# Optimization experiments

Hardware: AMD Instinct MI355X
Metric: run time of the kernel (lower is better)

The kernel has to match this reference:

```python
import jax, jax.numpy as jnp
import numpy as np

HIDDEN = 1024
N_HEADS = 16
HEAD_DIM = HIDDEN // N_HEADS


def _rope_tables(seq_len, dim, dtype):
    inv_freq = 1.0 / (10000.0 ** (jnp.arange(0, dim, 2, dtype=jnp.float32) / dim))
    t = jnp.arange(seq_len, dtype=jnp.float32)
    freqs = jnp.einsum('i,j->ij', t, inv_freq)          # [S, dim/2]
    emb = jnp.concatenate([freqs, freqs], axis=-1)       # [S, dim]
    cos = jnp.cos(emb)[None, :, None, :].astype(dtype)   # [1, S, 1, dim]
    sin = jnp.sin(emb)[None, :, None, :].astype(dtype)
    return cos, sin


def _rotate_half(x):
    x1, x2 = x[..., : x.shape[-1] // 2], x[..., x.shape[-1] // 2 :]
    return jnp.concatenate([-x2, x1], axis=-1)


def setup_inputs() -> dict:
    key = jax.random.key(0)
    ks = jax.random.split(key, 9)
    s = 1.0 / np.sqrt(HIDDEN)
    return {
        'x': jax.random.normal(ks[0], (2, 2048, HIDDEN), dtype=jnp.float32),
        'q_w': jax.random.uniform(ks[1], (HIDDEN, HIDDEN), jnp.float32, -s, s),
        'q_b': jax.random.uniform(ks[2], (HIDDEN,), jnp.float32, -s, s),
        'k_w': jax.random.uniform(ks[3], (HIDDEN, HIDDEN), jnp.float32, -s, s),
        'k_b': jax.random.uniform(ks[4], (HIDDEN,), jnp.float32, -s, s),
        'v_w': jax.random.uniform(ks[5], (HIDDEN, HIDDEN), jnp.float32, -s, s),
        'v_b': jax.random.uniform(ks[6], (HIDDEN,), jnp.float32, -s, s),
        'o_w': jax.random.uniform(ks[7], (HIDDEN, HIDDEN), jnp.float32, -s, s),
        'o_b': jax.random.uniform(ks[8], (HIDDEN,), jnp.float32, -s, s),
    }


def reference(x, q_w, q_b, k_w, k_b, v_w, v_b, o_w, o_b):
    B, S, _ = x.shape
    scale = HEAD_DIM ** -0.5
    # projections (torch Linear: x @ W.T + b)
    q = (x @ q_w.T + q_b).reshape(B, S, N_HEADS, HEAD_DIM)
    k = (x @ k_w.T + k_b).reshape(B, S, N_HEADS, HEAD_DIM)
    v = (x @ v_w.T + v_b).reshape(B, S, N_HEADS, HEAD_DIM)
    # RoPE
    cos, sin = _rope_tables(S, HEAD_DIM, x.dtype)
    q = q * cos + _rotate_half(q) * sin
    k = k * cos + _rotate_half(k) * sin
    # attention: [B, H, S, S]
    scores = jnp.einsum('bqhd,bkhd->bhqk', q, k) * scale
    attn = jax.nn.softmax(scores, axis=-1)
    out = jnp.einsum('bhqk,bkhd->bqhd', attn, v).reshape(B, S, HIDDEN)
    return out @ o_w.T + o_b
```

## Files before the change

### kernel.cpp

```cpp
#include <hip/hip_runtime.h>
#include <hip/hip_bf16.h>


#define SEQ    2048
#define BATCH  2
#define NHEADS 16
#define HDIM   64
#define HID    1024
#define NTOK   (BATCH*SEQ)

typedef __bf16 bf16x8 __attribute__((ext_vector_type(8)));
typedef float  f32x4  __attribute__((ext_vector_type(4)));
typedef float  f32x16 __attribute__((ext_vector_type(16)));
typedef unsigned short u16x8 __attribute__((ext_vector_type(8)));
typedef unsigned int   u32x4 __attribute__((ext_vector_type(4)));

__device__ __forceinline__ unsigned short bfc(float x) {
  return __builtin_bit_cast(unsigned short, (__bf16)x);
}
__device__ __forceinline__ unsigned int pk(float lo, float hi) {
  return (unsigned int)bfc(lo) | ((unsigned int)bfc(hi) << 16);
}
__device__ __forceinline__ void plswap(unsigned int& a, unsigned int& b) {
  asm volatile("v_permlane32_swap_b32 %0, %1" : "+v"(a), "+v"(b));
}
#define EXP2(x) __builtin_amdgcn_exp2f(x)
#define MFMA32(a, b, c) __builtin_amdgcn_mfma_f32_32x32x16_bf16(a, b, c, 0, 0, 0)

__device__ __forceinline__ void gload16(const void* gptr, void* ldsptr) {
  typedef __attribute__((address_space(3))) unsigned int as3_uint;
  typedef const __attribute__((address_space(1))) unsigned int as1_uint;
  __builtin_amdgcn_global_load_lds(
      (as1_uint*)(unsigned long long)gptr,
      (as3_uint*)(unsigned int)(unsigned long long)ldsptr,
      16, 0, 0);
}

__device__ __forceinline__ void cvt8(const float* __restrict__ s,
                                     unsigned short* __restrict__ d, int i) {
  float4 a = *reinterpret_cast<const float4*>(s + i);
  float4 b = *reinterpret_cast<const float4*>(s + i + 4);
  u16x8 o;
  o[0] = bfc(a.x); o[1] = bfc(a.y); o[2] = bfc(a.z); o[3] = bfc(a.w);
  o[4] = bfc(b.x); o[5] = bfc(b.y); o[6] = bfc(b.z); o[7] = bfc(b.w);
  *reinterpret_cast<u16x8*>(d + i) = o;
}

__global__ __launch_bounds__(256) void prep(
    const float* __restrict__ x,
    const float* __restrict__ qw, const float* __restrict__ kw,
    const float* __restrict__ vw, const float* __restrict__ ow,
    unsigned short* __restrict__ xb,
    unsigned short* __restrict__ wqb, unsigned short* __restrict__ wkb,
    unsigned short* __restrict__ wvb, unsigned short* __restrict__ wob,
    float* __restrict__ ct, float* __restrict__ st)
{
  const int XN = NTOK * HID / 8;
  const int WN = HID * HID / 8;
  int tid = blockIdx.x * 256 + threadIdx.x;
  if (tid < XN) {
    cvt8(x, xb, tid * 8);
  } else if (tid < XN + 4 * WN) {
    int r = tid - XN;
    int which = r >> 17;
    int i = (r & (WN - 1)) * 8;
    const float* s = (which == 0) ? qw : (which == 1) ? kw : (which == 2) ? vw : ow;
    unsigned short* d = (which == 0) ? wqb : (which == 1) ? wkb : (which == 2) ? wvb : wob;
    cvt8(s, d, i);
  } else {
    int idx = tid - (XN + 4 * WN);
    if (idx < SEQ * 32) {
      int p = idx >> 5, j = idx & 31;
      float inv = powf(10000.0f, -(float)(2 * j) * (1.0f / 64.0f));
      float a = (float)p * inv;
      ct[idx] = cosf(a);
      st[idx] = sinf(a);
    }
  }
}

__global__ __launch_bounds__(256) void gemm_qkv(
    const unsigned short* __restrict__ X,
    const unsigned short* __restrict__ Wq, const unsigned short* __restrict__ Wk,
    const unsigned short* __restrict__ Wv,
    const float* __restrict__ bq, const float* __restrict__ bk, const float* __restrict__ bv,
    const float* __restrict__ ct, const float* __restrict__ st,
    unsigned short* __restrict__ Qo, unsigned short* __restrict__ Ko,
    unsigned short* __restrict__ VTo)
{
  __shared__ unsigned short LSH[24576];
  const int z = blockIdx.z;
  const unsigned short* W = (z == 0) ? Wq : (z == 1) ? Wk : Wv;
  const float* bias = (z == 0) ? bq : (z == 1) ? bk : bv;
  const int tm = blockIdx.x, tn = blockIdx.y;
  const int t = threadIdx.x, w = t >> 6, l = t & 63;
  const int wm = w >> 1, wn = w & 1, g = l >> 4;

  f32x4 acc[4][4] = {};

  const int arow0 = tm * 128, brow0 = tn * 128;
  const int s0 = w * 2, s1 = w * 2 + 1;
  const int r0 = s0 * 16 + (l >> 2), r1 = s1 * 16 + (l >> 2);
  const int kc = (l & 3) * 8;

#define GSTAGE(buf, k0)                                                               \
  {                                                                                   \
    gload16(X + (long)(arow0 + r0) * HID + (k0) + kc, LSH + (buf) * 4096 + s0 * 512); \
    gload16(X + (long)(arow0 + r1) * HID + (k0) + kc, LSH + (buf) * 4096 + s1 * 512); \
    gload16(W + (long)(brow0 + r0) * HID + (k0) + kc, LSH + 12288 + (buf) * 4096 + s0 * 512); \
    gload16(W + (long)(brow0 + r1) * HID + (k0) + kc, LSH + 12288 + (buf) * 4096 + s1 * 512); \
  }

  GSTAGE(0, 0)
  GSTAGE(1, 32)
  asm volatile("s_waitcnt vmcnt(4)" ::: "memory");
  __builtin_amdgcn_s_barrier();
  int cur = 0, stg = 2;
  for (int k0 = 0; k0 < HID; k0 += 32) {
    if (k0 + 64 < HID) GSTAGE(stg, k0 + 64)
    bf16x8 af[4], bfr[4];
#pragma unroll
    for (int fm = 0; fm < 4; ++fm)
      af[fm] = *reinterpret_cast<const bf16x8*>(
          LSH + cur * 4096 + (wm * 64 + fm * 16 + (l & 15)) * 32 + g * 8);
#pragma unroll
    for (int fn = 0; fn < 4; ++fn)
      bfr[fn] = *reinterpret_cast<const bf16x8*>(
          LSH + 12288 + cur * 4096 + (wn * 64 + fn * 16 + (l & 15)) * 32 + g * 8);
    __builtin_amdgcn_s_setprio(1);
#pragma unroll
    for (int fm = 0; fm < 4; ++fm)
#pragma unroll
      for (int fn = 0; fn < 4; ++fn)
        acc[fm][fn] = __builtin_amdgcn_mfma_f32_16x16x32_bf16(af[fm], bfr[fn], acc[fm][fn], 0, 0, 0);
    __builtin_amdgcn_s_setprio(0);
    if (k0 + 64 < HID) {
      asm volatile("s_waitcnt vmcnt(4)" ::: "memory");
    } else {
      asm volatile("s_waitcnt vmcnt(0)" ::: "memory");
    }
    __builtin_amdgcn_s_barrier();
    cur = (cur == 2) ? 0 : cur + 1;
    stg = (stg == 2) ? 0 : stg + 1;
  }
#undef GSTAGE

  const int colb = brow0 + wn * 64;
  float bsv[4];
#pragma unroll
  for (int fn = 0; fn < 4; ++fn) bsv[fn] = bias[colb + fn * 16 + (l & 15)];

  if (z == 2) {
#pragma unroll
    for (int fm = 0; fm < 4; ++fm) {
      int tok = wm * 64 + fm * 16 + g * 4;
#pragma unroll
      for (int fn = 0; fn < 4; ++fn) {
        int col = wn * 64 + fn * 16 + (l & 15);
        unsigned int u0 = (unsigned int)bfc(acc[fm][fn][0] + bsv[fn]) |
                          ((unsigned int)bfc(acc[fm][fn][1] + bsv[fn]) << 16);
        unsigned int u1 = (unsigned int)bfc(acc[fm][fn][2] + bsv[fn]) |
                          ((unsigned int)bfc(acc[fm][fn][3] + bsv[fn]) << 16);
        uint2 uv; uv.x = u0; uv.y = u1;
        *reinterpret_cast<uint2*>(&LSH[col * 128 + (tok ^ ((col & 7) << 3))]) = uv;
      }
    }
    __syncthreads();
    const int bb = arow0 >> 11, stok = arow0 & (SEQ - 1);
#pragma unroll
    for (int p8 = 0; p8 < 8; ++p8) {
      int col = p8 * 16 + (t >> 4);
      int soff = (t & 15) * 8;
      uint4 v = *reinterpret_cast<const uint4*>(&LSH[col * 128 + (soff ^ ((col & 7) << 3))]);
      int hh = (brow0 + col) >> 6;
      int dd = col & 63;
      unsigned short* dst = VTo + ((long)(bb * NHEADS + hh) * HDIM + dd) * SEQ + stok + soff;
      *reinterpret_cast<uint4*>(dst) = v;
    }
    return;
  }

  unsigned short* Out = (z == 0) ? Qo : Ko;
  const int h = colb >> 6;
#pragma unroll
  for (int fm = 0; fm < 4; ++fm) {
#pragma unroll
    for (int r = 0; r < 4; ++r) {
      int grow = arow0 + wm * 64 + fm * 16 + g * 4 + r;
      int b = grow >> 11, sidx = grow & (SEQ - 1);
      unsigned short* ob = Out + ((long)(b * NHEADS + h) * SEQ + sidx) * HDIM;
#pragma unroll
      for (int fn2 = 0; fn2 < 2; ++fn2) {
        int d1 = fn2 * 16 + (l & 15);
        float v1 = acc[fm][fn2][r] + bsv[fn2];
        float v2 = acc[fm][fn2 + 2][r] + bsv[fn2 + 2];
        float c = ct[sidx * 32 + d1], sn = st[sidx * 32 + d1];
        float o1 = v1 * c - v2 * sn;
        float o2 = v2 * c + v1 * sn;
        if (z == 0) { o1 *= 0.18033688f; o2 *= 0.18033688f; }
        ob[d1] = bfc(o1);
        ob[d1 + 32] = bfc(o2);
      }
    }
  }
}

__global__ __launch_bounds__(256, 2) void attn(
    const unsigned short* __restrict__ Qb,
    const unsigned short* __restrict__ Kb,
    const unsigned short* __restrict__ VTb,
    unsigned short* __restrict__ Ob)
{
  __shared__ unsigned short Kl[4][64 * 64];
  __shared__ unsigned short Vl[4][64 * 64];
  const int bh = blockIdx.x, qt = blockIdx.y;
  const int b = bh >> 4, h = bh & 15;
  const int t = threadIdx.x, w = t >> 6, l = t & 63;
  const long hb = (long)bh * SEQ * HDIM;
  const int hh = l >> 5;
  const int swz = (l & 7) << 4;

  const int q0 = qt * 128 + w * 32;
  bf16x8 qf[4];
#pragma unroll
  for (int dc = 0; dc < 4; ++dc)
    qf[dc] = *reinterpret_cast<const bf16x8*>(
        Qb + hb + (long)(q0 + (l & 31)) * HDIM + dc * 16 + hh * 8);

  f32x16 oacc[2] = {};
  f32x16 oaccE = {};
  const f32x16 FZ16 = {};

  u32x4 ou; ou[0] = 0x3F803F80u; ou[1] = 0x3F803F80u; ou[2] = 0x3F803F80u; ou[3] = 0x3F803F80u;
  const bf16x8 ones8 = __builtin_bit_cast(bf16x8, ou);

  const int srow = l >> 3;
  const int scol = (((l & 7) * 16) ^ ((l >> 3) << 4)) >> 1;
  const unsigned short* kp0 = Kb + hb + (long)(w * 16 + srow) * HDIM + scol;
  const unsigned short* kp1 = kp0 + 8 * HDIM;
  const unsigned short* vp0 = VTb + hb + (long)(w * 16 + srow) * SEQ + scol;
  const unsigned short* vp1 = vp0 + 8 * SEQ;

#define STAGE(buf)                                                     \
  {                                                                    \
    gload16(kp0, (char*)Kl + (buf) * 8192 + w * 2048);                 \
    gload16(kp1, (char*)Kl + (buf) * 8192 + w * 2048 + 1024);          \
    gload16(vp0, (char*)Vl + (buf) * 8192 + w * 2048);                 \
    gload16(vp1, (char*)Vl + (buf) * 8192 + w * 2048 + 1024);          \
    kp0 += 64 * HDIM; kp1 += 64 * HDIM; vp0 += 64; vp1 += 64;          \
  }

#define QK(kbuf)                                                                  \
  _Pragma("unroll")                                                               \
  for (int blk = 0; blk < 2; ++blk) {                                             \
    const char* kb_ = (char*)Kl + (kbuf) * 8192 + (32 * blk + (l & 31)) * 128;    \
    bf16x8 kf0 = *reinterpret_cast<const bf16x8*>(kb_ + ((0 * 32 + hh * 16) ^ swz)); \
    sa[blk] = MFMA32(kf0, qf[0], FZ16);                                           \
    bf16x8 kf1 = *reinterpret_cast<const bf16x8*>(kb_ + ((1 * 32 + hh * 16) ^ swz)); \
    sa[blk] = MFMA32(kf1, qf[1], sa[blk]);                                        \
    bf16x8 kf2 = *reinterpret_cast<const bf16x8*>(kb_ + ((2 * 32 + hh * 16) ^ swz)); \
    sa[blk] = MFMA32(kf2, qf[2], sa[blk]);                                        \
    bf16x8 kf3 = *reinterpret_cast<const bf16x8*>(kb_ + ((3 * 32 + hh * 16) ^ swz)); \
    sa[blk] = MFMA32(kf3, qf[3], sa[blk]);                                        \
  }

#define SOFTEXP                                                                   \
  _Pragma("unroll")                                                               \
  for (int blk = 0; blk < 2; ++blk)                                               \
    _Pragma("unroll")                                                             \
    for (int r = 0; r < 16; ++r) sa[blk][r] = EXP2(sa[blk][r]);

#define PBUILD                                                                    \
  _Pragma("unroll")                                                               \
  for (int blk = 0; blk < 2; ++blk) {                                             \
    unsigned int w0a = pk(sa[blk][0], sa[blk][1]);                                \
    unsigned int w1a = pk(sa[blk][2], sa[blk][3]);                                \
    unsigned int w0b = pk(sa[blk][4], sa[blk][5]);                                \
    unsigned int w1b = pk(sa[blk][6], sa[blk][7]);                                \
    unsigned int w0c = pk(sa[blk][8], sa[blk][9]);                                \
    unsigned int w1c = pk(sa[blk][10], sa[blk][11]);                              \
    unsigned int w0d = pk(sa[blk][12], sa[blk][13]);                              \
    unsigned int w1d = pk(sa[blk][14], sa[blk][15]);                              \
    plswap(w0a, w0b); plswap(w1a, w1b);                                           \
    plswap(w0c, w0d); plswap(w1c, w1d);                                           \
    u32x4 f0; f0[0] = w0a; f0[1] = w1a; f0[2] = w0b; f0[3] = w1b;                 \
    u32x4 f1; f1[0] = w0c; f1[1] = w1c; f1[2] = w0d; f1[3] = w1d;                 \
    pB[2 * blk + 0] = __builtin_bit_cast(bf16x8, f0);                             \
    pB[2 * blk + 1] = __builtin_bit_cast(bf16x8, f1);                             \
  }

#define PVSTEP(vbuf)                                                              \
  _Pragma("unroll")                                                               \
  for (int db = 0; db < 2; ++db) {                                                \
    const char* vb_ = (char*)Vl + (vbuf) * 8192 + (32 * db + (l & 31)) * 128;     \
    _Pragma("unroll")                                                             \
    for (int kc = 0; kc < 4; ++kc) {                                              \
      bf16x8 vf = *reinterpret_cast<const bf16x8*>(vb_ + ((kc * 32 + hh * 16) ^ swz)); \
      oacc[db] = MFMA32(vf, pB[kc], oacc[db]);                                    \
    }                                                                             \
  }                                                                               \
  _Pragma("unroll")                                                               \
  for (int kc = 0; kc < 4; ++kc) oaccE = MFMA32(ones8, pB[kc], oaccE);

#define ITER(KB, VR, SW)                                   \
  {                                                        \
    STAGE(SW)                                              \
    __builtin_amdgcn_s_setprio(1);                         \
    QK(KB)                                                 \
    PVSTEP(VR)                                             \
    __builtin_amdgcn_s_setprio(0);                         \
    SOFTEXP                                                \
    PBUILD                                                 \
    asm volatile("s_waitcnt vmcnt(4)" ::: "memory");       \
    __builtin_amdgcn_s_barrier();                          \
  }
#define ITER_DRAIN(KB, VR)                                 \
  {                                                        \
    __builtin_amdgcn_s_setprio(1);                         \
    QK(KB)                                                 \
    PVSTEP(VR)                                             \
    __builtin_amdgcn_s_setprio(0);                         \
    SOFTEXP                                                \
    PBUILD                                                 \
    asm volatile("s_waitcnt vmcnt(0)" ::: "memory");       \
    __builtin_amdgcn_s_barrier();                          \
  }
#define ITER_LAST(KB, VR)                                  \
  {                                                        \
    __builtin_amdgcn_s_setprio(1);                         \
    QK(KB)                                                 \
    PVSTEP(VR)                                             \
    __builtin_amdgcn_s_setprio(0);                         \
    SOFTEXP                                                \
    PBUILD                                                 \
  }

  f32x16 sa[2];
  bf16x8 pB[4];

  STAGE(0)
  STAGE(1)
  asm volatile("s_waitcnt vmcnt(4)" ::: "memory");
  __builtin_amdgcn_s_barrier();

  STAGE(2)
  __builtin_amdgcn_s_setprio(1);
  QK(0)
  __builtin_amdgcn_s_setprio(0);
  SOFTEXP
  PBUILD
  asm volatile("s_waitcnt vmcnt(4)" ::: "memory");
  __builtin_amdgcn_s_barrier();

  for (int m = 0; m < 7; ++m) {
    ITER(1, 0, 3)
    ITER(2, 1, 0)
    ITER(3, 2, 1)
    ITER(0, 3, 2)
  }
  ITER(1, 0, 3)
  ITER_DRAIN(2, 1)
  ITER_LAST(3, 2)

  __builtin_amdgcn_s_setprio(1);
  PVSTEP(3)
  __builtin_amdgcn_s_setprio(0);

#undef STAGE
#undef QK
#undef SOFTEXP
#undef PBUILD
#undef PVSTEP
#undef ITER
#undef ITER_DRAIN
#undef ITER_LAST

  {
    float inv = 1.0f / oaccE[0];
    int q = q0 + (l & 31);
    unsigned short* op = Ob + (long)(b * SEQ + q) * HID + h * HDIM;
#pragma unroll
    for (int db = 0; db < 2; ++db)
#pragma unroll
      for (int a = 0; a < 4; ++a) {
        int d = 8 * a + 4 * hh + 32 * db;
        unsigned int lo = pk(oacc[db][4 * a + 0] * inv, oacc[db][4 * a + 1] * inv);
        unsigned int hi2 = pk(oacc[db][4 * a + 2] * inv, oacc[db][4 * a + 3] * inv);
        uint2 uv; uv.x = lo; uv.y = hi2;
        *reinterpret_cast<uint2*>(op + d) = uv;
      }
  }
}

__global__ __launch_bounds__(256) void gemm_o(
    const unsigned short* __restrict__ A,
    const unsigned short* __restrict__ W,
    const float* __restrict__ bias,
    float* __restrict__ Out)
{
  __shared__ unsigned short Al[3][128 * 32];
  __shared__ unsigned short Bl[3][64 * 32];
  const int tm = blockIdx.x, tn = blockIdx.y;
  const int t = threadIdx.x, w = t >> 6, l = t & 63;
  const int wm = w >> 1, wn = w & 1;

  f32x4 acc[4][2] = {};
  const int arow0 = tm * 128, brow0 = tn * 64;
  const int s0 = w * 2, s1 = w * 2 + 1;
  const int r0 = s0 * 16 + (l >> 2), r1 = s1 * 16 + (l >> 2);
  const int rb = w * 16 + (l >> 2);
  const int kc = (l & 3) * 8;

#define GSTAGE(buf, k0)                                                       \
  {                                                                           \
    gload16(A + (long)(arow0 + r0) * HID + (k0) + kc, Al[buf] + s0 * 512);    \
    gload16(A + (long)(arow0 + r1) * HID + (k0) + kc, Al[buf] + s1 * 512);    \
    gload16(W + (long)(brow0 + rb) * HID + (k0) + kc, Bl[buf] + w * 512);     \
  }

  GSTAGE(0, 0)
  GSTAGE(1, 32)
  asm volatile("s_waitcnt vmcnt(3)" ::: "memory");
  __builtin_amdgcn_s_barrier();
  int cur = 0, stg = 2;
  for (int k0 = 0; k0 < HID; k0 += 32) {
    if (k0 + 64 < HID) GSTAGE(stg, k0 + 64)
    bf16x8 af[4], bfr[2];
#pragma unroll
    for (int fm = 0; fm < 4; ++fm)
      af[fm] = *reinterpret_cast<const bf16x8*>(Al[cur] + (wm * 64 + fm * 16 + (l & 15)) * 32 + (l >> 4) * 8);
#pragma unroll
    for (int fn = 0; fn < 2; ++fn)
      bfr[fn] = *reinterpret_cast<const bf16x8*>(Bl[cur] + (wn * 32 + fn * 16 + (l & 15)) * 32 + (l >> 4) * 8);
    __builtin_amdgcn_s_setprio(1);
#pragma unroll
    for (int fm = 0; fm < 4; ++fm)
#pragma unroll
      for (int fn = 0; fn < 2; ++fn)
        acc[fm][fn] = __builtin_amdgcn_mfma_f32_16x16x32_bf16(af[fm], bfr[fn], acc[fm][fn], 0, 0, 0);
    __builtin_amdgcn_s_setprio(0);
    if (k0 + 64 < HID) {
      asm volatile("s_waitcnt vmcnt(3)" ::: "memory");
    } else {
      asm volatile("s_waitcnt vmcnt(0)" ::: "memory");
    }
    __builtin_amdgcn_s_barrier();
    cur = (cur == 2) ? 0 : cur + 1;
    stg = (stg == 2) ? 0 : stg + 1;
  }
#undef GSTAGE

  const int colb = brow0 + wn * 32;
  float bsv[2];
#pragma unroll
  for (int fn = 0; fn < 2; ++fn) bsv[fn] = bias[colb + fn * 16 + (l & 15)];
#pragma unroll
  for (int fm = 0; fm < 4; ++fm)
#pragma unroll
    for (int r = 0; r < 4; ++r) {
      int grow = arow0 + wm * 64 + fm * 16 + (l >> 4) * 4 + r;
#pragma unroll
      for (int fn = 0; fn < 2; ++fn)
        Out[(long)grow * HID + colb + fn * 16 + (l & 15)] = acc[fm][fn][r] + bsv[fn];
    }
}

extern "C" void kernel_launch(void* const* d_in, const int* in_sizes, int n_in,
                              void* d_out, int out_size, void* d_ws, size_t ws_size,
                              hipStream_t stream) {
  const float* x  = (const float*)d_in[0];
  const float* qw = (const float*)d_in[1];
  const float* qb = (const float*)d_in[2];
  const float* kw = (const float*)d_in[3];
  const float* kb = (const float*)d_in[4];
  const float* vw = (const float*)d_in[5];
  const float* vb = (const float*)d_in[6];
  const float* ow = (const float*)d_in[7];
  const float* ob = (const float*)d_in[8];
  float* out = (float*)d_out;

  char* p = (char*)d_ws;
  unsigned short* xb  = (unsigned short*)p; p += (size_t)NTOK * HID * 2;
  unsigned short* wqb = (unsigned short*)p; p += (size_t)HID * HID * 2;
  unsigned short* wkb = (unsigned short*)p; p += (size_t)HID * HID * 2;
  unsigned short* wvb = (unsigned short*)p; p += (size_t)HID * HID * 2;
  unsigned short* wob = (unsigned short*)p; p += (size_t)HID * HID * 2;
  unsigned short* Qb  = (unsigned short*)p; p += (size_t)NTOK * HID * 2;
  unsigned short* Kb  = (unsigned short*)p; p += (size_t)NTOK * HID * 2;
  unsigned short* VTb = (unsigned short*)p; p += (size_t)NTOK * HID * 2;
  float* ct = (float*)p; p += (size_t)SEQ * 32 * 4;
  float* st = (float*)p; p += (size_t)SEQ * 32 * 4;
  unsigned short* Ab  = xb;

  const int XN = NTOK * HID / 8, WN = HID * HID / 8;
  const int prep_threads = XN + 4 * WN + SEQ * 32;
  prep<<<dim3((prep_threads + 255) / 256), 256, 0, stream>>>(
      x, qw, kw, vw, ow, xb, wqb, wkb, wvb, wob, ct, st);

  gemm_qkv<<<dim3(NTOK / 128, HID / 128, 3), 256, 0, stream>>>(
      xb, wqb, wkb, wvb, qb, kb, vb, ct, st, Qb, Kb, VTb);

  attn<<<dim3(BATCH * NHEADS, SEQ / 128), 256, 0, stream>>>(Qb, Kb, VTb, Ab);

  gemm_o<<<dim3(NTOK / 128, HID / 64), 256, 0, stream>>>(Ab, wob, ob, out);
}
```

Baseline: 113.7 us.

## Shrink attention blocks to 64 queries with two waves and 2K/3V buffering

```diff
diff --git a/kernel.cpp b/kernel.cpp
--- a/kernel.cpp
+++ b/kernel.cpp
@@ -205,14 +205,14 @@
   }
 }
 
-__global__ __launch_bounds__(256, 2) void attn(
+__global__ __launch_bounds__(128, 2) void attn(
     const unsigned short* __restrict__ Qb,
     const unsigned short* __restrict__ Kb,
     const unsigned short* __restrict__ VTb,
     unsigned short* __restrict__ Ob)
 {
-  __shared__ unsigned short Kl[4][64 * 64];
-  __shared__ unsigned short Vl[4][64 * 64];
+  __shared__ unsigned short Kl[2][64 * 64];
+  __shared__ unsigned short Vl[3][64 * 64];
   const int bh = blockIdx.x, qt = blockIdx.y;
   const int b = bh >> 4, h = bh & 15;
   const int t = threadIdx.x, w = t >> 6, l = t & 63;
@@ -220,7 +220,7 @@
   const int hh = l >> 5;
   const int swz = (l & 7) << 4;
 
-  const int q0 = qt * 128 + w * 32;
+  const int q0 = qt * 64 + w * 32;
   bf16x8 qf[4];
 #pragma unroll
   for (int dc = 0; dc < 4; ++dc)
@@ -236,18 +236,18 @@
 
   const int srow = l >> 3;
   const int scol = (((l & 7) * 16) ^ ((l >> 3) << 4)) >> 1;
-  const unsigned short* kp0 = Kb + hb + (long)(w * 16 + srow) * HDIM + scol;
-  const unsigned short* kp1 = kp0 + 8 * HDIM;
-  const unsigned short* vp0 = VTb + hb + (long)(w * 16 + srow) * SEQ + scol;
-  const unsigned short* vp1 = vp0 + 8 * SEQ;
-
-#define STAGE(buf)                                                     \
-  {                                                                    \
-    gload16(kp0, (char*)Kl + (buf) * 8192 + w * 2048);                 \
-    gload16(kp1, (char*)Kl + (buf) * 8192 + w * 2048 + 1024);          \
-    gload16(vp0, (char*)Vl + (buf) * 8192 + w * 2048);                 \
-    gload16(vp1, (char*)Vl + (buf) * 8192 + w * 2048 + 1024);          \
-    kp0 += 64 * HDIM; kp1 += 64 * HDIM; vp0 += 64; vp1 += 64;          \
+  const unsigned short* kp0 = Kb + hb + (long)(w * 32 + srow) * HDIM + scol;
+  const unsigned short* vp0 = VTb + hb + (long)(w * 32 + srow) * SEQ + scol;
+
+#define STAGE(kb_, vb_)                                                       \
+  {                                                                           \
+    _Pragma("unroll")                                                         \
+    for (int c = 0; c < 4; ++c)                                               \
+      gload16(kp0 + c * 8 * HDIM, (char*)Kl + (kb_) * 8192 + w * 4096 + c * 1024); \
+    _Pragma("unroll")                                                         \
+    for (int c = 0; c < 4; ++c)                                               \
+      gload16(vp0 + c * 8 * SEQ, (char*)Vl + (vb_) * 8192 + w * 4096 + c * 1024);  \
+    kp0 += 64 * HDIM; vp0 += 64;                                              \
   }
 
 #define QK(kbuf)                                                                  \
@@ -302,20 +302,9 @@
   _Pragma("unroll")                                                               \
   for (int kc = 0; kc < 4; ++kc) oaccE = MFMA32(ones8, pB[kc], oaccE);
 
-#define ITER(KB, VR, SW)                                   \
+#define ITER(KB, VR, VW)                                   \
   {                                                        \
-    STAGE(SW)                                              \
-    __builtin_amdgcn_s_setprio(1);                         \
-    QK(KB)                                                 \
-    PVSTEP(VR)                                             \
-    __builtin_amdgcn_s_setprio(0);                         \
-    SOFTEXP                                                \
-    PBUILD                                                 \
-    asm volatile("s_waitcnt vmcnt(4)" ::: "memory");       \
-    __builtin_amdgcn_s_barrier();                          \
-  }
-#define ITER_DRAIN(KB, VR)                                 \
-  {                                                        \
+    STAGE((KB) ^ 1, VW)                                    \
     __builtin_amdgcn_s_setprio(1);                         \
     QK(KB)                                                 \
     PVSTEP(VR)                                             \
@@ -325,7 +314,7 @@
     asm volatile("s_waitcnt vmcnt(0)" ::: "memory");       \
     __builtin_amdgcn_s_barrier();                          \
   }
-#define ITER_LAST(KB, VR)                                  \
+#define ITER_NOSTAGE(KB, VR)                               \
   {                                                        \
     __builtin_amdgcn_s_setprio(1);                         \
     QK(KB)                                                 \
@@ -338,32 +327,31 @@
   f32x16 sa[2];
   bf16x8 pB[4];
 
-  STAGE(0)
-  STAGE(1)
-  asm volatile("s_waitcnt vmcnt(4)" ::: "memory");
+  STAGE(1 ^ 1, 0)
+  asm volatile("s_waitcnt vmcnt(0)" ::: "memory");
   __builtin_amdgcn_s_barrier();
 
-  STAGE(2)
+  STAGE(0 ^ 1, 1)
   __builtin_amdgcn_s_setprio(1);
   QK(0)
   __builtin_amdgcn_s_setprio(0);
   SOFTEXP
   PBUILD
-  asm volatile("s_waitcnt vmcnt(4)" ::: "memory");
+  asm volatile("s_waitcnt vmcnt(0)" ::: "memory");
   __builtin_amdgcn_s_barrier();
 
-  for (int m = 0; m < 7; ++m) {
-    ITER(1, 0, 3)
-    ITER(2, 1, 0)
-    ITER(3, 2, 1)
-    ITER(0, 3, 2)
-  }
-  ITER(1, 0, 3)
-  ITER_DRAIN(2, 1)
-  ITER_LAST(3, 2)
+  for (int m = 0; m < 5; ++m) {
+    ITER(1, 0, 2)
+    ITER(0, 1, 0)
+    ITER(1, 2, 1)
+    ITER(0, 0, 2)
+    ITER(1, 1, 0)
+    ITER(0, 2, 1)
+  }
+  ITER_NOSTAGE(1, 0)
 
   __builtin_amdgcn_s_setprio(1);
-  PVSTEP(3)
+  PVSTEP(1)
   __builtin_amdgcn_s_setprio(0);
 
 #undef STAGE
@@ -372,8 +360,7 @@
 #undef PBUILD
 #undef PVSTEP
 #undef ITER
-#undef ITER_DRAIN
-#undef ITER_LAST
+#undef ITER_NOSTAGE
 
   {
     float inv = 1.0f / oaccE[0];
@@ -500,7 +487,7 @@
   gemm_qkv<<<dim3(NTOK / 128, HID / 128, 3), 256, 0, stream>>>(
       xb, wqb, wkb, wvb, qb, kb, vb, ct, st, Qb, Kb, VTb);
 
-  attn<<<dim3(BATCH * NHEADS, SEQ / 128), 256, 0, stream>>>(Qb, Kb, VTb, Ab);
+  attn<<<dim3(BATCH * NHEADS, SEQ / 64), 128, 0, stream>>>(Qb, Kb, VTb, Ab);
 
   gemm_o<<<dim3(NTOK / 128, HID / 64), 256, 0, stream>>>(Ab, wob, ob, out);
 }
```

Measured after the change: 116.5 us. 1.02x slower.
